# Optimization experiments

Hardware: AMD Instinct MI355X
Metric: run time of the kernel (lower is better)

Reference implementation:

```python
import jax, jax.numpy as jnp
import numpy as np

# norse LIFParameters defaults with v_th overridden to 0.23
DT = 1e-3
TAU_SYN_INV = 200.0   # 1/5e-3
TAU_MEM_INV = 100.0   # 1/1e-2
V_TH = 0.23
ENC_V_TH = 1.0        # encoder uses default LIFParameters (v_th=1.0)
SEQ_LEN = 24
HIDDEN = 256
N_CLASSES = 10


def heaviside(x):
    return (x > 0).astype(x.dtype)


def encode(x):
    """ConstantCurrentLIFEncoder: lif_current_encoder over SEQ_LEN steps. x: [B, F] -> [T, B, F] spikes."""
    def step(v, _):
        v = v + DT * TAU_MEM_INV * (x - v)          # dv = dt*tau_mem_inv*((v_leak - v) + I)
        z = heaviside(v - ENC_V_TH)
        v = (1.0 - z) * v                            # reset to v_reset = 0
        return v, z
    _, zs = jax.lax.scan(step, jnp.zeros_like(x), None, length=SEQ_LEN)
    return zs


def lif_ff_step(inp, v, i):
    """norse lif_feed_forward_step: decay v with old i, decay i, spike, reset, then add input to i."""
    v_dec = v + DT * TAU_MEM_INV * (i - v)           # v_leak = 0
    i_dec = i * (1.0 - DT * TAU_SYN_INV)
    z = heaviside(v_dec - V_TH)
    v_new = (1.0 - z) * v_dec                        # v_reset = 0
    i_new = i_dec + inp
    return z, v_new, i_new


def setup_inputs() -> dict:
    key = jax.random.key(0)
    ks = jax.random.split(key, 8)
    B, F = 4096, 1024
    def lin(k, fan_in, fan_out):
        bound = 1.0 / np.sqrt(fan_in)
        kw, kb = jax.random.split(k)
        W = jax.random.uniform(kw, (fan_out, fan_in), jnp.float32, -bound, bound)
        b = jax.random.uniform(kb, (fan_out,), jnp.float32, -bound, bound)
        return W, b
    x = jax.random.normal(ks[0], (B, F), jnp.float32)
    W1, b1 = lin(ks[1], F, HIDDEN)
    W2, b2 = lin(ks[2], HIDDEN, HIDDEN)
    W3, b3 = lin(ks[3], HIDDEN, HIDDEN)
    Wli = jax.random.normal(ks[4], (N_CLASSES, HIDDEN), jnp.float32) * np.sqrt(2.0 / HIDDEN)
    return {"x": x, "W1": W1, "b1": b1, "W2": W2, "b2": b2, "W3": W3, "b3": b3, "Wli": Wli}


def reference(x, W1, b1, W2, b2, W3, b3, Wli):
    # dropout layers are identity in eval mode
    enc = encode(x)                                   # [T, B, F]
    B = x.shape[0]
    z2 = lambda d: jnp.zeros((B, d), x.dtype)
    carry0 = (z2(HIDDEN), z2(HIDDEN), z2(HIDDEN), z2(HIDDEN), z2(HIDDEN), z2(HIDDEN),
              z2(N_CLASSES), z2(N_CLASSES))
    def step(c, z):
        v1, i1, v2, i2, v3, i3, vo, io = c
        o1, v1, i1 = lif_ff_step(z @ W1.T + b1, v1, i1)
        o2, v2, i2 = lif_ff_step(o1 @ W2.T + b2, v2, i2)
        o2 = o2 + o1                                  # residual
        o3, v3, i3 = lif_ff_step(o2 @ W3.T + b3, v3, i3)
        o3 = o3 + o2                                  # residual
        # LILinearCell li_step: v from old i, i decays then accumulates W @ input (no bias)
        vo = vo + DT * TAU_MEM_INV * (io - vo)
        io = io * (1.0 - DT * TAU_SYN_INV) + o3 @ Wli.T
        return (v1, i1, v2, i2, v3, i3, vo, io), vo
    _, voltages = jax.lax.scan(step, carry0, enc)     # [T, B, n_classes]
    return voltages[-1]                               # decode = last timestep
```

## Files before the change

### kernel.cpp

```cpp
#include <hip/hip_runtime.h>
#include <hip/hip_bf16.h>

#define FEAT   1024
#define HID    256
#define TSTEPS 24
#define NCLS   10

typedef unsigned int u32;
typedef unsigned long long u64;
typedef unsigned short u16;
typedef float v2f __attribute__((ext_vector_type(2)));

constexpr int OFF_W1T  = 0;
constexpr int OFF_W2T  = OFF_W1T + 1025*HID;
constexpr int OFF_W3T  = OFF_W2T + 257*HID;
constexpr int OFF_WLI  = OFF_W3T + 257*HID;
constexpr int OFF_B1   = OFF_WLI + NCLS*HID;
constexpr int OFF_B2   = OFF_B1 + HID;
constexpr int OFF_B3   = OFF_B2 + HID;

struct CoefT { float c[TSTEPS]; };
constexpr CoefT make_coef() {
    CoefT r{};
    double c = 0.0, p9 = 1.0;
    r.c[TSTEPS-1] = 0.0f;
    for (int u = TSTEPS-1; u > 0; u--) {
        c = 0.8 * c + 0.1 * p9;
        p9 *= 0.9;
        r.c[u-1] = (float)c;
    }
    return r;
}
__device__ constexpr CoefT COEF = make_coef();

__device__ __forceinline__ u32 detect_bf16(const void* __restrict__ x, u32 lane) {
    float v = __bfloat162float(((const __hip_bfloat16*)x)[lane]);
    u64 bad = __ballot(!(fabsf(v) < 100.0f));
    return bad == 0ull ? 1u : 0u;
}

__device__ __forceinline__ float rd_any(const void* p, int idx, u32 isbf) {
    return isbf ? __bfloat162float(((const __hip_bfloat16*)p)[idx])
                : ((const float*)p)[idx];
}

__device__ __forceinline__ float4 rd4(const void* p, int i, u32 isbf) {
    if (isbf) {
        const u32* q = (const u32*)p;
        u32 a = q[i >> 1], b = q[(i >> 1) + 1];
        float4 r;
        r.x = __uint_as_float(a << 16); r.y = __uint_as_float(a & 0xffff0000u);
        r.z = __uint_as_float(b << 16); r.w = __uint_as_float(b & 0xffff0000u);
        return r;
    }
    return ((const float4*)p)[i >> 2];
}

__global__ __launch_bounds__(256) void prep_k(const void* __restrict__ x,
        const void* W1, const void* W2, const void* W3, const void* Wli,
        const void* b1, const void* b2, const void* b3, float* __restrict__ ws) {
    const u32 isbf = detect_bf16(x, threadIdx.x & 63);
    const u32 t = threadIdx.x;
    int b = blockIdx.x;

    if (b == 384) {
        for (u32 e = t; e < NCLS*HID; e += 256) ws[OFF_WLI + e] = rd_any(Wli, e, isbf);
        ws[OFF_B1 + t] = rd_any(b1, t, isbf);
        ws[OFF_B2 + t] = rd_any(b2, t, isbf);
        ws[OFF_B3 + t] = rd_any(b3, t, isbf);
        ws[OFF_W1T + 1024*HID + t] = 0.f;
        ws[OFF_W2T + 256*HID + t] = 0.f;
        ws[OFF_W3T + 256*HID + t] = 0.f;
        return;
    }

    const void* src; float* dst; int srcW, h0, f0;
    if (b < 256)      { src = W1; dst = ws + OFF_W1T; srcW = FEAT; h0 = (b >> 5) * 32; f0 = (b & 31) * 32; }
    else if (b < 320) { int tb = b - 256; src = W2; dst = ws + OFF_W2T; srcW = HID; h0 = (tb >> 3) * 32; f0 = (tb & 7) * 32; }
    else              { int tb = b - 320; src = W3; dst = ws + OFF_W3T; srcW = HID; h0 = (tb >> 3) * 32; f0 = (tb & 7) * 32; }

    __shared__ float sm[32 * 36];
    {
        u32 r = t >> 3, c4 = (t & 7) * 4;
        float4 w = rd4(src, (h0 + r) * srcW + f0 + c4, isbf);
        *(float4*)&sm[r * 36 + c4] = w;
    }
    __syncthreads();
    {
        u32 f = t >> 3, h4 = (t & 7) * 4;
        float4 o;
        o.x = sm[(h4 + 0) * 36 + f];
        o.y = sm[(h4 + 1) * 36 + f];
        o.z = sm[(h4 + 2) * 36 + f];
        o.w = sm[(h4 + 3) * 36 + f];
        *(float4*)&dst[(size_t)(f0 + f) * HID + h0 + h4] = o;
    }
}

__device__ __forceinline__ u32 mbcnt64(u64 m) {
    return __builtin_amdgcn_mbcnt_hi((u32)(m >> 32),
           __builtin_amdgcn_mbcnt_lo((u32)m, 0u));
}


__device__ __forceinline__ u32 build_listE(u16* list, u32 lm, u32 lane) {
    u32 cnt = (u32)__builtin_popcount(lm);
    u32 pos = 0, n = 0;
    #pragma unroll
    for (int b = 0; b < 5; b++) {
        u64 B = __ballot(((cnt >> b) & 1u) != 0);
        pos += mbcnt64(B) << b;
        n += ((u32)__builtin_popcountll(B)) << b;
    }
    while (lm) {
        u32 j = (u32)__builtin_ctz(lm); lm &= lm - 1;
        list[pos++] = (u16)((lane << 4) + j);
    }
    u32 np = (n + 3u) & ~3u;
    if (lane < np - n) list[n + lane] = (u16)1024;
    return np;
}

__device__ __forceinline__ uint2 build_listZ(u16* list, u32 lm, u32 start, u32 lane) {
    u32 cnt = (u32)__builtin_popcount(lm);
    u64 B0 = __ballot((cnt & 1u) != 0);
    u64 B1 = __ballot((cnt & 2u) != 0);
    u64 B2 = __ballot((cnt & 4u) != 0);
    u32 pos = start + mbcnt64(B0) + 2u*mbcnt64(B1) + 4u*mbcnt64(B2);
    u32 n = start + (u32)__builtin_popcountll(B0) + 2u*(u32)__builtin_popcountll(B1)
          + 4u*(u32)__builtin_popcountll(B2);
    while (lm) {
        u32 j = (u32)__builtin_ctz(lm); lm &= lm - 1;
        list[pos++] = (u16)((lane << 2) + j);
    }
    u32 np = (n + 3u) & ~3u;
    if (lane < np - n) list[n + lane] = (u16)256;
    return make_uint2(n, np);
}

#define GADD(V) do { A += (v2f){(V).x, (V).y}; B += (v2f){(V).z, (V).w}; } while (0)

__device__ __forceinline__ void gather(v2f& A, v2f& B, const float* __restrict__ Wt,
                                       const u16* __restrict__ list, u32 np, u32 lane16) {
    const char* __restrict__ base = (const char*)Wt;
    u32 c = 0;
    for (; c + 8 <= np; c += 8) {
        uint4 d = *(const uint4*)(list + c);
        const float4 v0 = *(const float4*)(base + ((d.x & 0xffffu) << 10) + lane16);
        const float4 v1 = *(const float4*)(base + ((d.x >> 16)     << 10) + lane16);
        const float4 v2 = *(const float4*)(base + ((d.y & 0xffffu) << 10) + lane16);
        const float4 v3 = *(const float4*)(base + ((d.y >> 16)     << 10) + lane16);
        const float4 v4 = *(const float4*)(base + ((d.z & 0xffffu) << 10) + lane16);
        const float4 v5 = *(const float4*)(base + ((d.z >> 16)     << 10) + lane16);
        const float4 v6 = *(const float4*)(base + ((d.w & 0xffffu) << 10) + lane16);
        const float4 v7 = *(const float4*)(base + ((d.w >> 16)     << 10) + lane16);
        GADD(v0); GADD(v1); GADD(v2); GADD(v3);
        GADD(v4); GADD(v5); GADD(v6); GADD(v7);
    }
    if (c < np) {
        uint2 d = *(const uint2*)(list + c);
        const float4 v0 = *(const float4*)(base + ((d.x & 0xffffu) << 10) + lane16);
        const float4 v1 = *(const float4*)(base + ((d.x >> 16)     << 10) + lane16);
        const float4 v2 = *(const float4*)(base + ((d.y & 0xffffu) << 10) + lane16);
        const float4 v3 = *(const float4*)(base + ((d.y >> 16)     << 10) + lane16);
        GADD(v0); GADD(v1); GADD(v2); GADD(v3);
    }
}

__global__ __launch_bounds__(64) void snn_k(const void* __restrict__ xin,
                                            const float* __restrict__ ws,
                                            void* __restrict__ out) {
    const u32 lane = threadIdx.x;
    const int row  = blockIdx.x;
    const u32 lane16 = lane * 16;
    const u32 isbf = detect_bf16(xin, lane);

    const float* __restrict__ W1T = ws + OFF_W1T;
    const float* __restrict__ W2T = ws + OFF_W2T;
    const float* __restrict__ W3T = ws + OFF_W3T;
    const float* __restrict__ WLI = ws + OFF_WLI;

    __shared__ u32 sched[12 * 64];
    __shared__ __align__(16) u16 lE[1032];
    __shared__ __align__(16) u16 lL[520];

    {
        float xv[16];
        if (isbf) {
            const uint4* xp = (const uint4*)((const u16*)xin + (size_t)row*FEAT + lane*16);
            uint4 A = xp[0], B = xp[1];
            u32 w[8] = {A.x, A.y, A.z, A.w, B.x, B.y, B.z, B.w};
            #pragma unroll
            for (int i = 0; i < 8; i++) {
                xv[2*i]   = __uint_as_float(w[i] << 16);
                xv[2*i+1] = __uint_as_float(w[i] & 0xffff0000u);
            }
        } else {
            const float4* xp = (const float4*)((const float*)xin + (size_t)row*FEAT + lane*16);
            float4 A = xp[0], B = xp[1], C = xp[2], D = xp[3];
            float tmp[16] = {A.x,A.y,A.z,A.w,B.x,B.y,B.z,B.w,C.x,C.y,C.z,C.w,D.x,D.y,D.z,D.w};
            #pragma unroll
            for (int i = 0; i < 16; i++) xv[i] = tmp[i];
        }
        u32 smreg[12];
        #pragma unroll
        for (int i = 0; i < 12; i++) smreg[i] = 0;
        #pragma unroll
        for (int j = 0; j < 16; j++) {
            float v = 0.f;
            #pragma unroll
            for (int t = 0; t < TSTEPS; t++) {
                v = v + 0.1f * (xv[j] - v);
                bool z = v > 1.0f;
                v = z ? 0.0f : v;
                if (z) smreg[t >> 1] |= 1u << (((t & 1) << 4) + j);
            }
        }
        #pragma unroll
        for (int i = 0; i < 12; i++) sched[i * 64 + lane] = smreg[i];
    }

    float v1[4], i1[4], v2[4], i2[4], v3[4], i3[4], g[4];
    #pragma unroll
    for (int k = 0; k < 4; k++) {
        v1[k]=0.f; i1[k]=0.f; v2[k]=0.f; i2[k]=0.f; v3[k]=0.f; i3[k]=0.f; g[k]=0.f;
    }
    const u32 lane4 = lane * 4;
    const float4 b1v = *(const float4*)(ws + OFF_B1 + lane4);
    const float4 b2v = *(const float4*)(ws + OFF_B2 + lane4);
    const float4 b3v = *(const float4*)(ws + OFF_B3 + lane4);

    u32 pairreg = 0;
    for (int t = 0; t < TSTEPS; t++) {
        if ((t & 1) == 0) pairreg = sched[(t >> 1) * 64 + lane];
        const u32 lmE = (t & 1) ? (pairreg >> 16) : (pairreg & 0xffffu);

        u32 npE = build_listE(lE, lmE, lane);
        v2f accA = {b1v.x, b1v.y}, accB = {b1v.z, b1v.w};
        gather(accA, accB, W1T, lE, npE, lane16);
        float a1[4] = {accA.x, accA.y, accB.x, accB.y};

        float o1v[4]; u32 lm1 = 0;
        #pragma unroll
        for (int kk = 0; kk < 4; kk++) {
            float vd = v1[kk] + 0.1f * (i1[kk] - v1[kk]);
            i1[kk] = i1[kk] * 0.8f;
            bool z = vd > 0.23f;
            v1[kk] = z ? 0.0f : vd;
            i1[kk] = i1[kk] + a1[kk];
            o1v[kk] = z ? 1.0f : 0.0f;
            lm1 |= (z ? 1u : 0u) << kk;
        }

        uint2 r1 = build_listZ(lL, lm1, 0u, lane);
        accA = (v2f){b2v.x, b2v.y}; accB = (v2f){b2v.z, b2v.w};
        gather(accA, accB, W2T, lL, r1.y, lane16);
        float a2[4] = {accA.x, accA.y, accB.x, accB.y};

        float o2v[4]; u32 lm2 = 0;
        #pragma unroll
        for (int kk = 0; kk < 4; kk++) {
            float vd = v2[kk] + 0.1f * (i2[kk] - v2[kk]);
            i2[kk] = i2[kk] * 0.8f;
            bool z = vd > 0.23f;
            v2[kk] = z ? 0.0f : vd;
            i2[kk] = i2[kk] + a2[kk];
            o2v[kk] = (z ? 1.0f : 0.0f) + o1v[kk];
            lm2 |= (z ? 1u : 0u) << kk;
        }

        uint2 r2 = build_listZ(lL, lm2, r1.x, lane);
        v2f acc3A = {b3v.x, b3v.y}, acc3B = {b3v.z, b3v.w};
        gather(acc3A, acc3B, W3T, lL, r2.y, lane16);
        float a3[4] = {acc3A.x, acc3A.y, acc3B.x, acc3B.y};

        const float cf = COEF.c[t];
        #pragma unroll
        for (int kk = 0; kk < 4; kk++) {
            float vd = v3[kk] + 0.1f * (i3[kk] - v3[kk]);
            i3[kk] = i3[kk] * 0.8f;
            bool z = vd > 0.23f;
            v3[kk] = z ? 0.0f : vd;
            i3[kk] = i3[kk] + a3[kk];
            float o3 = (z ? 1.0f : 0.0f) + o2v[kk];
            g[kk] += cf * o3;
        }
    }

    float s[NCLS];
    #pragma unroll
    for (int c = 0; c < NCLS; c++) {
        const float4 w = *(const float4*)(WLI + c*HID + lane4);
        float p = g[0]*w.x + g[1]*w.y + g[2]*w.z + g[3]*w.w;
        #pragma unroll
        for (int d = 32; d > 0; d >>= 1) p += __shfl_xor(p, d, 64);
        s[c] = p;
    }
    if (lane == 0) {
        if (isbf) {
            __hip_bfloat16* o = (__hip_bfloat16*)out + (size_t)row*NCLS;
            #pragma unroll
            for (int c = 0; c < NCLS; c++) o[c] = __float2bfloat16(s[c]);
        } else {
            float* o = (float*)out + (size_t)row*NCLS;
            #pragma unroll
            for (int c = 0; c < NCLS; c++) o[c] = s[c];
        }
    }
}

extern "C" void kernel_launch(void* const* d_in, const int* in_sizes, int n_in,
                              void* d_out, int out_size, void* d_ws, size_t ws_size,
                              hipStream_t stream) {
    const void* x   = d_in[0];
    const void* W1  = d_in[1];
    const void* b1  = d_in[2];
    const void* W2  = d_in[3];
    const void* b2  = d_in[4];
    const void* W3  = d_in[5];
    const void* b3  = d_in[6];
    const void* Wli = d_in[7];
    float* ws = (float*)d_ws;
    const int batch = in_sizes[0] / FEAT;

    prep_k<<<385, 256, 0, stream>>>(x, W1, W2, W3, Wli, b1, b2, b3, ws);
    snn_k<<<batch, 64, 0, stream>>>(x, ws, d_out);
}
```

Measured before the change: 147.3 us.

## Fuse layer-2 and layer-3 sparse gathers over shared spike list, skip empty lists

The layer-1 spike list is now gathered once against both W2 and W3 in a single dual-gather loop. The layer-3 pass then only covers the new layer-2 spikes, instead of rebuilding and walking the combined list. Each list build and gather is skipped when no lane in the wave has spikes, and list padding shrinks from multiples of 4 to multiples of 2 so fewer zero-row loads are issued. Risk: the layer-3 gather now starts at an offset that is only 4-byte aligned while its main loop reads the list with 16-byte vector loads, which could be misaligned LDS accesses.

```diff
diff --git a/kernel.cpp b/kernel.cpp
--- a/kernel.cpp
+++ b/kernel.cpp
@@ -116,12 +116,12 @@
         u32 j = (u32)__builtin_ctz(lm); lm &= lm - 1;
         list[pos++] = (u16)((lane << 4) + j);
     }
-    u32 np = (n + 3u) & ~3u;
-    if (lane < np - n) list[n + lane] = (u16)1024;
+    u32 np = (n + 1u) & ~1u;
+    if (lane == 0 && np != n) list[n] = (u16)1024;
     return np;
 }
 
-__device__ __forceinline__ uint2 build_listZ(u16* list, u32 lm, u32 start, u32 lane) {
+__device__ __forceinline__ u32 build_listZ(u16* list, u32 lm, u32 start, u32 lane) {
     u32 cnt = (u32)__builtin_popcount(lm);
     u64 B0 = __ballot((cnt & 1u) != 0);
     u64 B1 = __ballot((cnt & 2u) != 0);
@@ -133,12 +133,12 @@
         u32 j = (u32)__builtin_ctz(lm); lm &= lm - 1;
         list[pos++] = (u16)((lane << 2) + j);
     }
-    u32 np = (n + 3u) & ~3u;
-    if (lane < np - n) list[n + lane] = (u16)256;
-    return make_uint2(n, np);
-}
-
-#define GADD(V) do { A += (v2f){(V).x, (V).y}; B += (v2f){(V).z, (V).w}; } while (0)
+    u32 np = (n + 1u) & ~1u;
+    if (lane == 0 && np != n) list[n] = (u16)256;
+    return np;
+}
+
+#define GADD(AA, BB, V) do { AA += (v2f){(V).x, (V).y}; BB += (v2f){(V).z, (V).w}; } while (0)
 
 __device__ __forceinline__ void gather(v2f& A, v2f& B, const float* __restrict__ Wt,
                                        const u16* __restrict__ list, u32 np, u32 lane16) {
@@ -154,16 +154,47 @@
         const float4 v5 = *(const float4*)(base + ((d.z >> 16)     << 10) + lane16);
         const float4 v6 = *(const float4*)(base + ((d.w & 0xffffu) << 10) + lane16);
         const float4 v7 = *(const float4*)(base + ((d.w >> 16)     << 10) + lane16);
-        GADD(v0); GADD(v1); GADD(v2); GADD(v3);
-        GADD(v4); GADD(v5); GADD(v6); GADD(v7);
-    }
-    if (c < np) {
+        GADD(A, B, v0); GADD(A, B, v1); GADD(A, B, v2); GADD(A, B, v3);
+        GADD(A, B, v4); GADD(A, B, v5); GADD(A, B, v6); GADD(A, B, v7);
+    }
+    for (; c < np; c += 2) {
+        u32 d = *(const u32*)(list + c);
+        const float4 v0 = *(const float4*)(base + ((d & 0xffffu) << 10) + lane16);
+        const float4 v1 = *(const float4*)(base + ((d >> 16)     << 10) + lane16);
+        GADD(A, B, v0); GADD(A, B, v1);
+    }
+}
+
+__device__ __forceinline__ void gather_dual(v2f& A2, v2f& B2, v2f& A3, v2f& B3,
+        const float* __restrict__ W2t, const float* __restrict__ W3t,
+        const u16* __restrict__ list, u32 np, u32 lane16) {
+    const char* __restrict__ b2 = (const char*)W2t;
+    const char* __restrict__ b3 = (const char*)W3t;
+    u32 c = 0;
+    for (; c + 4 <= np; c += 4) {
         uint2 d = *(const uint2*)(list + c);
-        const float4 v0 = *(const float4*)(base + ((d.x & 0xffffu) << 10) + lane16);
-        const float4 v1 = *(const float4*)(base + ((d.x >> 16)     << 10) + lane16);
-        const float4 v2 = *(const float4*)(base + ((d.y & 0xffffu) << 10) + lane16);
-        const float4 v3 = *(const float4*)(base + ((d.y >> 16)     << 10) + lane16);
-        GADD(v0); GADD(v1); GADD(v2); GADD(v3);
+        u32 o0 = (d.x & 0xffffu) << 10, o1 = (d.x >> 16) << 10;
+        u32 o2 = (d.y & 0xffffu) << 10, o3 = (d.y >> 16) << 10;
+        const float4 a0 = *(const float4*)(b2 + o0 + lane16);
+        const float4 a1 = *(const float4*)(b2 + o1 + lane16);
+        const float4 a2 = *(const float4*)(b2 + o2 + lane16);
+        const float4 a3 = *(const float4*)(b2 + o3 + lane16);
+        const float4 c0 = *(const float4*)(b3 + o0 + lane16);
+        const float4 c1 = *(const float4*)(b3 + o1 + lane16);
+        const float4 c2 = *(const float4*)(b3 + o2 + lane16);
+        const float4 c3 = *(const float4*)(b3 + o3 + lane16);
+        GADD(A2, B2, a0); GADD(A2, B2, a1); GADD(A2, B2, a2); GADD(A2, B2, a3);
+        GADD(A3, B3, c0); GADD(A3, B3, c1); GADD(A3, B3, c2); GADD(A3, B3, c3);
+    }
+    for (; c < np; c += 2) {
+        u32 d = *(const u32*)(list + c);
+        u32 o0 = (d & 0xffffu) << 10, o1 = (d >> 16) << 10;
+        const float4 a0 = *(const float4*)(b2 + o0 + lane16);
+        const float4 a1 = *(const float4*)(b2 + o1 + lane16);
+        const float4 c0 = *(const float4*)(b3 + o0 + lane16);
+        const float4 c1 = *(const float4*)(b3 + o1 + lane16);
+        GADD(A2, B2, a0); GADD(A2, B2, a1);
+        GADD(A3, B3, c0); GADD(A3, B3, c1);
     }
 }
 
@@ -235,9 +266,11 @@
         if ((t & 1) == 0) pairreg = sched[(t >> 1) * 64 + lane];
         const u32 lmE = (t & 1) ? (pairreg >> 16) : (pairreg & 0xffffu);
 
-        u32 npE = build_listE(lE, lmE, lane);
         v2f accA = {b1v.x, b1v.y}, accB = {b1v.z, b1v.w};
-        gather(accA, accB, W1T, lE, npE, lane16);
+        if (__ballot(lmE != 0u)) {
+            u32 npE = build_listE(lE, lmE, lane);
+            gather(accA, accB, W1T, lE, npE, lane16);
+        }
         float a1[4] = {accA.x, accA.y, accB.x, accB.y};
 
         float o1v[4]; u32 lm1 = 0;
@@ -252,10 +285,14 @@
             lm1 |= (z ? 1u : 0u) << kk;
         }
 
-        uint2 r1 = build_listZ(lL, lm1, 0u, lane);
-        accA = (v2f){b2v.x, b2v.y}; accB = (v2f){b2v.z, b2v.w};
-        gather(accA, accB, W2T, lL, r1.y, lane16);
-        float a2[4] = {accA.x, accA.y, accB.x, accB.y};
+        v2f acc2A = {b2v.x, b2v.y}, acc2B = {b2v.z, b2v.w};
+        v2f acc3A = {b3v.x, b3v.y}, acc3B = {b3v.z, b3v.w};
+        u32 np1 = 0;
+        if (__ballot(lm1 != 0u)) {
+            np1 = build_listZ(lL, lm1, 0u, lane);
+            gather_dual(acc2A, acc2B, acc3A, acc3B, W2T, W3T, lL, np1, lane16);
+        }
+        float a2[4] = {acc2A.x, acc2A.y, acc2B.x, acc2B.y};
 
         float o2v[4]; u32 lm2 = 0;
         #pragma unroll
@@ -269,9 +306,10 @@
             lm2 |= (z ? 1u : 0u) << kk;
         }
 
-        uint2 r2 = build_listZ(lL, lm2, r1.x, lane);
-        v2f acc3A = {b3v.x, b3v.y}, acc3B = {b3v.z, b3v.w};
-        gather(acc3A, acc3B, W3T, lL, r2.y, lane16);
+        if (__ballot(lm2 != 0u)) {
+            u32 np2 = build_listZ(lL, lm2, np1, lane);
+            gather(acc3A, acc3B, W3T, lL + np1, np2 - np1, lane16);
+        }
         float a3[4] = {acc3A.x, acc3A.y, acc3B.x, acc3B.y};
 
         const float cf = COEF.c[t];
```

Result: faster. 144.0 us (-2.2%).
